# Optimization experiments

Hardware: AMD Instinct MI355X
Metric: run time of the kernel (lower is better)

## Reference

```python
import jax, jax.numpy as jnp
import numpy as np

N_BASIS = 5  # identity, transpose, diag-embed(diag), row-sum broadcast, total-sum broadcast


def eq2to2_ops(x):
    """x: [B, d, n, n] -> [B, 5, d, n, n] equivariant basis ops (sums normalized by n, n^2)."""
    n = x.shape[-1]
    eye = jnp.eye(n, dtype=x.dtype)
    xt = jnp.swapaxes(x, -1, -2)
    diag = jnp.diagonal(x, axis1=-2, axis2=-1)            # [B, d, n]
    diag_emb = diag[..., :, None] * eye                   # [B, d, n, n]
    row = jnp.broadcast_to(x.sum(-1, keepdims=True) / n, x.shape)
    tot = jnp.broadcast_to(x.sum((-2, -1), keepdims=True) / (n * n), x.shape)
    return jnp.stack([x, xt, diag_emb, row, tot], axis=1)


def eq_layer(x, W, b):
    """x: [B, d_in, n, n]; W: [d_in, d_out, 5]; b: [d_out] -> [B, d_out, n, n]."""
    ops = eq2to2_ops(x)                                   # [B, 5, d_in, n, n]
    return jnp.einsum('bqdij,dsq->bsij', ops, W) + b[None, :, None, None]


def setup_inputs() -> dict:
    key = jax.random.key(0)
    ks = jax.random.split(key, 8)
    B, n, nin, nhid, ndechid, nout = 8, 256, 16, 32, 128, 1
    s = lambda fan: 1.0 / np.sqrt(fan)
    return {
        'x': jax.random.normal(ks[0], (B, n, nin), jnp.float32),
        'W1': jax.random.normal(ks[1], (2 * nin, nhid, N_BASIS), jnp.float32) * s(2 * nin * N_BASIS),
        'b1': jnp.zeros((nhid,), jnp.float32),
        'W2': jax.random.normal(ks[2], (nhid, nhid, N_BASIS), jnp.float32) * s(nhid * N_BASIS),
        'b2': jnp.zeros((nhid,), jnp.float32),
        'D1': jax.random.normal(ks[3], (nhid, ndechid), jnp.float32) * s(nhid),
        'db1': jnp.zeros((ndechid,), jnp.float32),
        'D2': jax.random.normal(ks[4], (ndechid, ndechid), jnp.float32) * s(ndechid),
        'db2': jnp.zeros((ndechid,), jnp.float32),
        'D3': jax.random.normal(ks[5], (ndechid, nout), jnp.float32) * s(ndechid),
        'db3': jnp.zeros((nout,), jnp.float32),
    }


def reference(x, W1, b1, W2, b2, D1, db1, D2, db2, D3, db3):
    B, n, d = x.shape
    eye = jnp.eye(n, dtype=x.dtype)
    # diag_embed(x.permute(0,2,1)) -> [B, d, n, n]
    x1 = jnp.swapaxes(x, 1, 2)[..., :, None] * eye
    # outer-product pairwise interactions -> [B, d, n, n]
    x2 = jnp.einsum('bid,bjd->bdij', x, x)
    h = jnp.concatenate([x1, x2], axis=1)                 # [B, 2d, n, n]
    h = jax.nn.relu(eq_layer(h, W1, b1))
    h = jax.nn.relu(eq_layer(h, W2, b2))
    h = jax.nn.relu(h.sum((-2, -1)))                      # [B, nhid]
    h = jax.nn.relu(h @ D1 + db1)
    h = jax.nn.relu(h @ D2 + db2)
    return h @ D3 + db3
```

## Files before the change

kernel.cpp:

```cpp
#include <hip/hip_runtime.h>
#include <hip/hip_bf16.h>


#define NB 8
#define NN 256
#define ND 16
#define NC 32
#define W1S 160
#define W2S 160
#define XP 20

using bf16x8 = __attribute__((ext_vector_type(8))) __bf16;
using f32x4  = __attribute__((ext_vector_type(4))) float;

#define MFMA(a, b, c) __builtin_amdgcn_mfma_f32_16x16x32_bf16((a), (b), (c), 0, 0, 0)

#define WAVE_LDS_SYNC() do {                      \
    __builtin_amdgcn_wave_barrier();              \
    __builtin_amdgcn_s_waitcnt(0xc07f);  \
    __builtin_amdgcn_wave_barrier();              \
} while (0)

__device__ __forceinline__ bf16x8 make_av(const float* xi, const float* xj, int quad)
{
    bf16x8 av;
    if (quad < 2) {
        const float4* a = (const float4*)(xi + quad * 8);
        const float4* b = (const float4*)(xj + quad * 8);
        float4 a0 = a[0], a1 = a[1], b0 = b[0], b1 = b[1];
        av[0] = (__bf16)(a0.x * b0.x); av[1] = (__bf16)(a0.y * b0.y);
        av[2] = (__bf16)(a0.z * b0.z); av[3] = (__bf16)(a0.w * b0.w);
        av[4] = (__bf16)(a1.x * b1.x); av[5] = (__bf16)(a1.y * b1.y);
        av[6] = (__bf16)(a1.z * b1.z); av[7] = (__bf16)(a1.w * b1.w);
    } else {
        #pragma unroll
        for (int j = 0; j < 8; ++j) av[j] = (__bf16)0.f;
    }
    return av;
}

__device__ __forceinline__ unsigned pack2(float lo, float hi)
{
    union { __bf16 b[2]; unsigned u; } p;
    p.b[0] = (__bf16)lo; p.b[1] = (__bf16)hi;
    return p.u;
}

__global__ __launch_bounds__(256) void kC_rows(
    const float* __restrict__ x, const float* __restrict__ W1,
    const float* __restrict__ b1, const float* __restrict__ W2,
    float* __restrict__ T1g, float* __restrict__ R1, float* __restrict__ Dg1,
    float* __restrict__ TotP, float* __restrict__ CD2, float* __restrict__ CR2)
{
    const int TI = blockIdx.x, b = blockIdx.y, t = threadIdx.x;
    __shared__ __align__(16) float  sX[NN][XP];
    __shared__ __align__(16) __bf16 sBQ[NC][48];
    __shared__ float part[16][ND + 1];
    __shared__ float sS[ND];
    __shared__ float sRT[4][NC], sDgL[4][NC], sRow[4][NC], sDiag[4][NC];

    {
        const float4* xg4 = (const float4*)(x + b * NN * ND);
        #pragma unroll
        for (int kk = 0; kk < 4; ++kk) {
            int idx = t + kk * 256;
            int row = idx >> 2, c4 = idx & 3;
            *(float4*)&sX[row][c4 * 4] = xg4[idx];
        }
    }
    #pragma unroll
    for (int kk = 0; kk < 2; ++kk) {
        int idx = t + kk * 256; int c = idx >> 4, k = idx & 15;
        sBQ[c][k] = (__bf16)(W1[(ND + k) * W1S + c * 5 + 0]
                           + W1[(ND + k) * W1S + c * 5 + 1]);
    }
    #pragma unroll
    for (int kk = 0; kk < 4; ++kk) {
        int idx = t + kk * 256;
        sBQ[idx >> 5][16 + (idx & 31)] = (__bf16)0.f;
    }
    __syncthreads();

    {
        int rr = t >> 4, d = t & 15;
        float p = 0.f;
        #pragma unroll
        for (int k = 0; k < 16; ++k) p += sX[rr + (k << 4)][d];
        part[rr][d] = p;
    }
    __syncthreads();
    if (t < ND) {
        float s = 0.f;
        #pragma unroll
        for (int k = 0; k < 16; ++k) s += part[k][t];
        sS[t] = s;
    }
    __syncthreads();
    if (t < 128) {
        int i_l = t >> 5, c = t & 31;
        int gi = TI * 4 + i_l;
        float r = 0.f, dg = 0.f, tt = 0.f;
        #pragma unroll
        for (int d = 0; d < ND; ++d) {
            float xi = sX[gi][d], sd = sS[d];
            const float* wa = W1 + d * W1S + c * 5;
            const float* wb = W1 + (ND + d) * W1S + c * 5;
            r  += xi * wa[3] + xi * sd * wb[3];
            dg += xi * (wa[0] + wa[1] + wa[2]) + xi * xi * wb[2];
            tt += sd * wa[4] + sd * sd * wb[4];
        }
        r *= (1.f / 256.f);
        float t1 = tt * (1.f / 65536.f) + b1[c];
        R1[(b * NN + gi) * NC + c] = r;
        Dg1[(b * NN + gi) * NC + c] = dg;
        sRT[i_l][c] = t1 + r;
        sDgL[i_l][c] = dg;
        if (TI == 0 && i_l == 0) T1g[b * NC + c] = t1;
    }
    __syncthreads();

    const int ln = t & 63, wv = t >> 6;
    const int m = ln & 15, quad = ln >> 4;
    const int gi = TI * 4 + wv;
    bf16x8 bq0 = *(const bf16x8*)&sBQ[m][8 * quad];
    bf16x8 bq1 = *(const bf16x8*)&sBQ[m + 16][8 * quad];
    float rt0 = sRT[wv][m], rt1 = sRT[wv][m + 16];
    float dg0 = sDgL[wv][m], dg1 = sDgL[wv][m + 16];
    f32x4 zero = {0.f, 0.f, 0.f, 0.f};
    float rs0 = 0.f, rs1 = 0.f;

    for (int jg = 0; jg < 8; ++jg) {
        #pragma unroll
        for (int gg = 0; gg < 2; ++gg) {
            int jrow = jg * 32 + gg * 16 + m;
            bf16x8 av = make_av(&sX[gi][0], &sX[jrow][0], quad);
            f32x4 q0 = MFMA(av, bq0, zero);
            f32x4 q1 = MFMA(av, bq1, zero);
            int jb = jg * 32 + gg * 16 + quad * 4;
            #pragma unroll
            for (int r = 0; r < 4; ++r) {
                float v0 = q0[r] + rt0, v1 = q1[r] + rt1;
                bool dgf = (jb + r == gi);
                if (dgf) { v0 += dg0; v1 += dg1; }
                float h0 = fmaxf(v0, 0.f), h1 = fmaxf(v1, 0.f);
                if (dgf) { sDiag[wv][m] = h0; sDiag[wv][m + 16] = h1; }
                rs0 += h0; rs1 += h1;
            }
        }
    }
    rs0 += __shfl_down(rs0, 32, 64); rs0 += __shfl_down(rs0, 16, 64);
    rs1 += __shfl_down(rs1, 32, 64); rs1 += __shfl_down(rs1, 16, 64);
    if (ln < 16) { sRow[wv][ln] = rs0; sRow[wv][ln + 16] = rs1; }
    __syncthreads();
    if (t < NC)
        TotP[TI * (NB * NC) + b * NC + t]
            = sRow[0][t] + sRow[1][t] + sRow[2][t] + sRow[3][t];
    if (t < 128) {
        int i_l = t >> 5, s = t & 31;
        int gi2 = TI * 4 + i_l;
        float cd = 0.f, cr = 0.f;
        #pragma unroll
        for (int c = 0; c < NC; ++c) {
            cd += sDiag[i_l][c] * W2[c * W2S + s * 5 + 2];
            cr += sRow[i_l][c]  * W2[c * W2S + s * 5 + 3];
        }
        CD2[(b * NN + gi2) * NC + s] = cd;
        CR2[(b * NN + gi2) * NC + s] = cr * (1.f / 256.f);
    }
}

__global__ __launch_bounds__(256) void kD_main(
    const float* __restrict__ x, const float* __restrict__ W1,
    const float* __restrict__ W2, const float* __restrict__ b2,
    const float* __restrict__ T1g, const float* __restrict__ R1g,
    const float* __restrict__ Dg1g, const float* __restrict__ CD2g,
    const float* __restrict__ CR2g, const float* __restrict__ TotP,
    float* __restrict__ GP)
{
    const int b = blockIdx.y, t = threadIdx.x;
    int TI = 0, rem = blockIdx.x;
    while (rem >= 16 - TI) { rem -= 16 - TI; ++TI; }
    const int TJ = TI + rem;
    const bool diagblk = (TI == TJ), mirror = !diagblk;

    __shared__ __align__(16) __bf16 sUw[4][16][40];
    __shared__ __align__(16) __bf16 sVw[4][16][40];
    __shared__ __align__(16) __bf16 sBQ[NC][48];
    __shared__ __align__(16) __bf16 sWp[NC][40], sWm[NC][40];
    __shared__ __align__(16) float sXI[16][XP], sXJ[16][XP];
    __shared__ float sTot[NC], sCT2[NC];
    __shared__ float red[4][NC];

    if (t < 128) {
        const float4* xg4 = (const float4*)(x + b * NN * ND);
        int half = t >> 6, idx = t & 63;
        int row = idx >> 2, c4 = idx & 3;
        int base = (half ? TJ : TI) * 16;
        float4 v = xg4[(base + row) * 4 + c4];
        float* dst = half ? &sXJ[row][c4 * 4] : &sXI[row][c4 * 4];
        *(float4*)dst = v;
    }
    #pragma unroll
    for (int kk = 0; kk < 2; ++kk) {
        int idx = t + kk * 256; int c = idx >> 4, k = idx & 15;
        sBQ[c][k] = (__bf16)(W1[(ND + k) * W1S + c * 5 + 0]
                           + W1[(ND + k) * W1S + c * 5 + 1]);
    }
    #pragma unroll
    for (int kk = 0; kk < 4; ++kk) {
        int idx = t + kk * 256;
        sBQ[idx >> 5][16 + (idx & 31)] = (__bf16)0.f;
    }
    #pragma unroll
    for (int kk = 0; kk < 4; ++kk) {
        int idx = t + kk * 256; int s = idx >> 5, kp = idx & 31;
        int c = ((kp & 1) << 4) | (kp >> 1);
        float w0 = W2[c * W2S + s * 5 + 0], w1 = W2[c * W2S + s * 5 + 1];
        sWp[s][kp] = (__bf16)((w0 + w1) * 0.5f);
        sWm[s][kp] = (__bf16)((w0 - w1) * 0.5f);
    }
    if (t < NC) {
        float tot = 0.f;
        #pragma unroll
        for (int k = 0; k < 64; ++k) tot += TotP[k * (NB * NC) + b * NC + t];
        sTot[t] = tot;
    }
    if (t < 64) {
        WAVE_LDS_SYNC();
        if (t < NC) {
            float ct = 0.f;
            #pragma unroll
            for (int c = 0; c < NC; ++c) ct += sTot[c] * W2[c * W2S + t * 5 + 4];
            sCT2[t] = ct * (1.f / 65536.f) + b2[t];
        }
    }

    const int ln = t & 63, wv = t >> 6;
    const int m = ln & 15, quad = ln >> 4;

    const float* R1b = R1g + b * NN * NC;
    const float* Dgb = Dg1g + b * NN * NC;
    const float* CDb = CD2g + b * NN * NC;
    const float* CRb = CR2g + b * NN * NC;
    float t10 = T1g[b * NC + m], t11 = T1g[b * NC + m + 16];
    float rti[4][2], dgi[4][2], rtj[4][2];
    float cri[4][2], cdi[4][2], crj[4][2];
    #pragma unroll
    for (int gg = 0; gg < 4; ++gg) {
        int rowI = TI * 16 + wv * 4 + gg;
        rti[gg][0] = R1b[rowI * NC + m] + t10;
        rti[gg][1] = R1b[rowI * NC + m + 16] + t11;
        dgi[gg][0] = Dgb[rowI * NC + m];
        dgi[gg][1] = Dgb[rowI * NC + m + 16];
        cri[gg][0] = CRb[rowI * NC + m];
        cri[gg][1] = CRb[rowI * NC + m + 16];
        cdi[gg][0] = CDb[rowI * NC + m];
        cdi[gg][1] = CDb[rowI * NC + m + 16];
    }
    #pragma unroll
    for (int r = 0; r < 4; ++r) {
        int rowJ = TJ * 16 + quad * 4 + r;
        rtj[r][0] = R1b[rowJ * NC + m] + t10;
        rtj[r][1] = R1b[rowJ * NC + m + 16] + t11;
        crj[r][0] = CRb[rowJ * NC + m];
        crj[r][1] = CRb[rowJ * NC + m + 16];
    }
    __syncthreads();

    float ct0 = sCT2[m], ct1 = sCT2[m + 16];
    #pragma unroll
    for (int gg = 0; gg < 4; ++gg) { cri[gg][0] += ct0; cri[gg][1] += ct1; }
    #pragma unroll
    for (int r = 0; r < 4; ++r) { crj[r][0] += ct0; crj[r][1] += ct1; }

    bf16x8 bq0 = *(const bf16x8*)&sBQ[m][8 * quad];
    bf16x8 bq1 = *(const bf16x8*)&sBQ[m + 16][8 * quad];
    bf16x8 wp0 = *(const bf16x8*)&sWp[m][8 * quad];
    bf16x8 wp1 = *(const bf16x8*)&sWp[m + 16][8 * quad];
    bf16x8 wm0 = *(const bf16x8*)&sWm[m][8 * quad];
    bf16x8 wm1 = *(const bf16x8*)&sWm[m + 16][8 * quad];
    __bf16* Uw = &sUw[wv][0][0];
    __bf16* Vw = &sVw[wv][0][0];
    f32x4 zero = {0.f, 0.f, 0.f, 0.f};
    float acc0 = 0.f, acc1 = 0.f;

    #pragma unroll
    for (int gg = 0; gg < 4; ++gg) {
        int g = wv * 4 + gg;
        __builtin_amdgcn_wave_barrier();
        {
            bf16x8 av = make_av(&sXI[g][0], &sXJ[m][0], quad);
            f32x4 q0 = MFMA(av, bq0, zero);
            f32x4 q1 = MFMA(av, bq1, zero);
            #pragma unroll
            for (int r = 0; r < 4; ++r) {
                int tj = quad * 4 + r;
                float a0 = q0[r] + rti[gg][0], b0 = q0[r] + rtj[r][0];
                float a1 = q1[r] + rti[gg][1], b1 = q1[r] + rtj[r][1];
                if (diagblk && tj == g) {
                    a0 += dgi[gg][0]; b0 = a0;
                    a1 += dgi[gg][1]; b1 = a1;
                }
                float hA0 = fmaxf(a0, 0.f), hB0 = fmaxf(b0, 0.f);
                float hA1 = fmaxf(a1, 0.f), hB1 = fmaxf(b1, 0.f);
                *(unsigned*)&Uw[tj * 40 + 2 * m] = pack2(hA0 + hB0, hA1 + hB1);
                *(unsigned*)&Vw[tj * 40 + 2 * m] = pack2(hA0 - hB0, hA1 - hB1);
            }
        }
        WAVE_LDS_SYNC();
        {
            bf16x8 ua = *(const bf16x8*)&Uw[m * 40 + 8 * quad];
            bf16x8 va = *(const bf16x8*)&Vw[m * 40 + 8 * quad];
            f32x4 P0 = MFMA(ua, wp0, zero);
            f32x4 M0 = MFMA(va, wm0, zero);
            f32x4 P1 = MFMA(ua, wp1, zero);
            f32x4 M1 = MFMA(va, wm1, zero);
            #pragma unroll
            for (int r = 0; r < 4; ++r) {
                int tj = quad * 4 + r;
                float a1v = P0[r] + M0[r] + cri[gg][0];
                float a2v = P0[r] - M0[r] + crj[r][0];
                float e1 = P1[r] + M1[r] + cri[gg][1];
                float e2 = P1[r] - M1[r] + crj[r][1];
                if (diagblk && tj == g) { a1v += cdi[gg][0]; e1 += cdi[gg][1]; }
                acc0 += fmaxf(a1v, 0.f); acc1 += fmaxf(e1, 0.f);
                if (mirror) { acc0 += fmaxf(a2v, 0.f); acc1 += fmaxf(e2, 0.f); }
            }
        }
    }

    acc0 += __shfl_down(acc0, 32, 64); acc0 += __shfl_down(acc0, 16, 64);
    acc1 += __shfl_down(acc1, 32, 64); acc1 += __shfl_down(acc1, 16, 64);
    if (ln < 16) { red[wv][ln] = acc0; red[wv][ln + 16] = acc1; }
    __syncthreads();
    if (t < NC)
        GP[blockIdx.x * (NB * NC) + b * NC + t]
            = red[0][t] + red[1][t] + red[2][t] + red[3][t];
}

__global__ __launch_bounds__(256) void k5_mlp(
    const float* __restrict__ GP, const float* __restrict__ D1,
    const float* __restrict__ db1, const float* __restrict__ D2,
    const float* __restrict__ db2, const float* __restrict__ D3,
    const float* __restrict__ db3, float* __restrict__ out)
{
    int b = blockIdx.x, t = threadIdx.x;
    __shared__ float sGp[8][NC], a[NC], h2s[128], r2[2];
    {
        int q = t >> 5, s = t & 31;
        float p = 0.f;
        for (int k = q; k < 136; k += 8) p += GP[k * (NB * NC) + b * NC + s];
        sGp[q][s] = p;
    }
    __syncthreads();
    if (t < NC) {
        float s = 0.f;
        #pragma unroll
        for (int q = 0; q < 8; ++q) s += sGp[q][t];
        a[t] = fmaxf(s, 0.f);
    }
    __syncthreads();
    if (t < 128) {
        float acc = db1[t];
        #pragma unroll
        for (int s = 0; s < NC; ++s) acc += a[s] * D1[s * 128 + t];
        h2s[t] = fmaxf(acc, 0.f);
    }
    __syncthreads();
    if (t < 128) {
        float acc2 = db2[t];
        #pragma unroll 8
        for (int u = 0; u < 128; ++u) acc2 += h2s[u] * D2[u * 128 + t];
        float h3 = fmaxf(acc2, 0.f);
        float v = h3 * D3[t];
        #pragma unroll
        for (int off = 32; off > 0; off >>= 1) v += __shfl_down(v, off, 64);
        if ((t & 63) == 0) r2[t >> 6] = v;
    }
    __syncthreads();
    if (t == 0) out[b] = r2[0] + r2[1] + db3[0];
}

extern "C" void kernel_launch(void* const* d_in, const int* in_sizes, int n_in,
                              void* d_out, int out_size, void* d_ws, size_t ws_size,
                              hipStream_t stream)
{
    const float* x   = (const float*)d_in[0];
    const float* W1  = (const float*)d_in[1];
    const float* b1  = (const float*)d_in[2];
    const float* W2  = (const float*)d_in[3];
    const float* b2  = (const float*)d_in[4];
    const float* D1  = (const float*)d_in[5];
    const float* db1 = (const float*)d_in[6];
    const float* D2  = (const float*)d_in[7];
    const float* db2 = (const float*)d_in[8];
    const float* D3  = (const float*)d_in[9];
    const float* db3 = (const float*)d_in[10];
    float* out = (float*)d_out;

    float* w = (float*)d_ws;
    float* pT1   = w; w += NB * NC;
    float* pTotP = w; w += 64 * NB * NC;
    float* pGP   = w; w += 136 * NB * NC;
    float* pR1   = w; w += NB * NN * NC;
    float* pDg1  = w; w += NB * NN * NC;
    float* pCD2  = w; w += NB * NN * NC;
    float* pCR2  = w; w += NB * NN * NC;

    hipLaunchKernelGGL(kC_rows, dim3(64, NB), dim3(256), 0, stream,
                       x, W1, b1, W2, pT1, pR1, pDg1, pTotP, pCD2, pCR2);
    hipLaunchKernelGGL(kD_main, dim3(136, NB), dim3(256), 0, stream,
                       x, W1, W2, b2, pT1, pR1, pDg1, pCD2, pCR2, pTotP, pGP);
    hipLaunchKernelGGL(k5_mlp, dim3(NB), dim3(256), 0, stream,
                       pGP, D1, db1, D2, db2, D3, db3, out);
}
```

Before: 111.2 us.

## Fuse MLP tail into main kernel via last-block counter, precompute weight tiles

Removes the separate k5_mlp launch. The last block per batch to finish kD_main, detected with an atomic counter and release/acquire fences, now runs the MLP tail. The first kC_rows block precomputes the packed bf16 weight tiles (BQ, Wp/Wm, W2 slice 4) into workspace, so each kD_main block loads them with vector copies instead of rebuilding them from strided W2/W1 reads. kC_rows also stages W1 in shared memory for its per-row reductions. This adds atomics and a serialized tail in one block per batch, and extra shared memory in kC_rows.

```diff
diff --git a/kernel.cpp b/kernel.cpp
--- a/kernel.cpp
+++ b/kernel.cpp
@@ -9,6 +9,7 @@
 #define W1S 160
 #define W2S 160
 #define XP 20
+#define NBLK 136
 
 using bf16x8 = __attribute__((ext_vector_type(8))) __bf16;
 using f32x4  = __attribute__((ext_vector_type(4))) float;
@@ -50,10 +51,13 @@
     const float* __restrict__ x, const float* __restrict__ W1,
     const float* __restrict__ b1, const float* __restrict__ W2,
     float* __restrict__ T1g, float* __restrict__ R1, float* __restrict__ Dg1,
-    float* __restrict__ TotP, float* __restrict__ CD2, float* __restrict__ CR2)
+    float* __restrict__ TotP, float* __restrict__ CD2, float* __restrict__ CR2,
+    __bf16* __restrict__ BQt, __bf16* __restrict__ Wpm,
+    float* __restrict__ Wt4, int* __restrict__ Cnt)
 {
     const int TI = blockIdx.x, b = blockIdx.y, t = threadIdx.x;
     __shared__ __align__(16) float  sX[NN][XP];
+    __shared__ __align__(16) float  sW1[2 * ND][W1S];
     __shared__ __align__(16) __bf16 sBQ[NC][48];
     __shared__ float part[16][ND + 1];
     __shared__ float sS[ND];
@@ -68,6 +72,12 @@
             *(float4*)&sX[row][c4 * 4] = xg4[idx];
         }
     }
+    {
+        const float4* wg1 = (const float4*)W1;
+        float4* sw1 = (float4*)&sW1[0][0];
+        #pragma unroll
+        for (int kk = 0; kk < 5; ++kk) sw1[t + kk * 256] = wg1[t + kk * 256];
+    }
     #pragma unroll
     for (int kk = 0; kk < 2; ++kk) {
         int idx = t + kk * 256; int c = idx >> 4, k = idx & 15;
@@ -88,6 +98,19 @@
         for (int k = 0; k < 16; ++k) p += sX[rr + (k << 4)][d];
         part[rr][d] = p;
     }
+    if (TI == 0 && b == 0) {
+        if (t < 192) ((float4*)BQt)[t] = ((const float4*)&sBQ[0][0])[t];
+        for (int idx = t; idx < 1024; idx += 256) {
+            int s = idx >> 5, kp = idx & 31;
+            int c = ((kp & 1) << 4) | (kp >> 1);
+            float w0 = W2[c * W2S + s * 5 + 0], w1 = W2[c * W2S + s * 5 + 1];
+            Wpm[s * 40 + kp]        = (__bf16)((w0 + w1) * 0.5f);
+            Wpm[1280 + s * 40 + kp] = (__bf16)((w0 - w1) * 0.5f);
+        }
+        for (int idx = t; idx < 1024; idx += 256)
+            Wt4[(idx >> 5) * 32 + (idx & 31)] = W2[(idx >> 5) * W2S + (idx & 31) * 5 + 4];
+        if (t < NB) Cnt[t] = 0;
+    }
     __syncthreads();
     if (t < ND) {
         float s = 0.f;
@@ -103,8 +126,8 @@
         #pragma unroll
         for (int d = 0; d < ND; ++d) {
             float xi = sX[gi][d], sd = sS[d];
-            const float* wa = W1 + d * W1S + c * 5;
-            const float* wb = W1 + (ND + d) * W1S + c * 5;
+            const float* wa = &sW1[d][c * 5];
+            const float* wb = &sW1[ND + d][c * 5];
             r  += xi * wa[3] + xi * sd * wb[3];
             dg += xi * (wa[0] + wa[1] + wa[2]) + xi * xi * wb[2];
             tt += sd * wa[4] + sd * sd * wb[4];
@@ -170,12 +193,17 @@
 }
 
 __global__ __launch_bounds__(256) void kD_main(
-    const float* __restrict__ x, const float* __restrict__ W1,
-    const float* __restrict__ W2, const float* __restrict__ b2,
+    const float* __restrict__ x,
+    const __bf16* __restrict__ BQt, const __bf16* __restrict__ Wpm,
+    const float* __restrict__ Wt4, const float* __restrict__ b2,
     const float* __restrict__ T1g, const float* __restrict__ R1g,
     const float* __restrict__ Dg1g, const float* __restrict__ CD2g,
     const float* __restrict__ CR2g, const float* __restrict__ TotP,
-    float* __restrict__ GP)
+    float* __restrict__ GP, int* __restrict__ Cnt,
+    const float* __restrict__ D1, const float* __restrict__ db1,
+    const float* __restrict__ D2, const float* __restrict__ db2,
+    const float* __restrict__ D3, const float* __restrict__ db3,
+    float* __restrict__ out)
 {
     const int b = blockIdx.y, t = threadIdx.x;
     int TI = 0, rem = blockIdx.x;
@@ -190,6 +218,8 @@
     __shared__ __align__(16) float sXI[16][XP], sXJ[16][XP];
     __shared__ float sTot[NC], sCT2[NC];
     __shared__ float red[4][NC];
+    __shared__ int sLast;
+    __shared__ float sGp[8][NC], sA[NC], h2s[128], r2[2];
 
     if (t < 128) {
         const float4* xg4 = (const float4*)(x + b * NN * ND);
@@ -200,24 +230,15 @@
         float* dst = half ? &sXJ[row][c4 * 4] : &sXI[row][c4 * 4];
         *(float4*)dst = v;
     }
-    #pragma unroll
-    for (int kk = 0; kk < 2; ++kk) {
-        int idx = t + kk * 256; int c = idx >> 4, k = idx & 15;
-        sBQ[c][k] = (__bf16)(W1[(ND + k) * W1S + c * 5 + 0]
-                           + W1[(ND + k) * W1S + c * 5 + 1]);
-    }
-    #pragma unroll
-    for (int kk = 0; kk < 4; ++kk) {
-        int idx = t + kk * 256;
-        sBQ[idx >> 5][16 + (idx & 31)] = (__bf16)0.f;
-    }
-    #pragma unroll
-    for (int kk = 0; kk < 4; ++kk) {
-        int idx = t + kk * 256; int s = idx >> 5, kp = idx & 31;
-        int c = ((kp & 1) << 4) | (kp >> 1);
-        float w0 = W2[c * W2S + s * 5 + 0], w1 = W2[c * W2S + s * 5 + 1];
-        sWp[s][kp] = (__bf16)((w0 + w1) * 0.5f);
-        sWm[s][kp] = (__bf16)((w0 - w1) * 0.5f);
+    if (t < 192) ((float4*)&sBQ[0][0])[t] = ((const float4*)BQt)[t];
+    {
+        const float4* wsrc = (const float4*)Wpm;
+        #pragma unroll
+        for (int i = t; i < 320; i += 256) {
+            float4 v = wsrc[i];
+            if (i < 160) ((float4*)&sWp[0][0])[i] = v;
+            else         ((float4*)&sWm[0][0])[i - 160] = v;
+        }
     }
     if (t < NC) {
         float tot = 0.f;
@@ -230,7 +251,7 @@
         if (t < NC) {
             float ct = 0.f;
             #pragma unroll
-            for (int c = 0; c < NC; ++c) ct += sTot[c] * W2[c * W2S + t * 5 + 4];
+            for (int c = 0; c < NC; ++c) ct += sTot[c] * Wt4[c * 32 + t];
             sCT2[t] = ct * (1.f / 65536.f) + b2[t];
         }
     }
@@ -336,20 +357,24 @@
     if (t < NC)
         GP[blockIdx.x * (NB * NC) + b * NC + t]
             = red[0][t] + red[1][t] + red[2][t] + red[3][t];
-}
-
-__global__ __launch_bounds__(256) void k5_mlp(
-    const float* __restrict__ GP, const float* __restrict__ D1,
-    const float* __restrict__ db1, const float* __restrict__ D2,
-    const float* __restrict__ db2, const float* __restrict__ D3,
-    const float* __restrict__ db3, float* __restrict__ out)
-{
-    int b = blockIdx.x, t = threadIdx.x;
-    __shared__ float sGp[8][NC], a[NC], h2s[128], r2[2];
+
+    __builtin_amdgcn_fence(__ATOMIC_RELEASE, "agent");
+    if (t == 0) {
+        int old = __hip_atomic_fetch_add(Cnt + b, 1, __ATOMIC_RELAXED,
+                                         __HIP_MEMORY_SCOPE_AGENT);
+        sLast = (old == NBLK - 1) ? 1 : 0;
+    }
+    __syncthreads();
+    if (!sLast) return;
+    __builtin_amdgcn_fence(__ATOMIC_ACQUIRE, "agent");
+
     {
         int q = t >> 5, s = t & 31;
         float p = 0.f;
-        for (int k = q; k < 136; k += 8) p += GP[k * (NB * NC) + b * NC + s];
+        #pragma unroll
+        for (int k = q; k < NBLK; k += 8)
+            p += __hip_atomic_load(&GP[k * (NB * NC) + b * NC + s],
+                                   __ATOMIC_RELAXED, __HIP_MEMORY_SCOPE_AGENT);
         sGp[q][s] = p;
     }
     __syncthreads();
@@ -357,13 +382,13 @@
         float s = 0.f;
         #pragma unroll
         for (int q = 0; q < 8; ++q) s += sGp[q][t];
-        a[t] = fmaxf(s, 0.f);
+        sA[t] = fmaxf(s, 0.f);
     }
     __syncthreads();
     if (t < 128) {
         float acc = db1[t];
         #pragma unroll
-        for (int s = 0; s < NC; ++s) acc += a[s] * D1[s * 128 + t];
+        for (int s = 0; s < NC; ++s) acc += sA[s] * D1[s * 128 + t];
         h2s[t] = fmaxf(acc, 0.f);
     }
     __syncthreads();
@@ -401,16 +426,20 @@
     float* w = (float*)d_ws;
     float* pT1   = w; w += NB * NC;
     float* pTotP = w; w += 64 * NB * NC;
-    float* pGP   = w; w += 136 * NB * NC;
+    float* pGP   = w; w += NBLK * NB * NC;
     float* pR1   = w; w += NB * NN * NC;
     float* pDg1  = w; w += NB * NN * NC;
     float* pCD2  = w; w += NB * NN * NC;
     float* pCR2  = w; w += NB * NN * NC;
+    __bf16* pBQt = (__bf16*)w; w += 768;
+    __bf16* pWpm = (__bf16*)w; w += 1280;
+    float* pWt4  = w; w += 1024;
+    int*   pCnt  = (int*)w; w += 8;
 
     hipLaunchKernelGGL(kC_rows, dim3(64, NB), dim3(256), 0, stream,
-                       x, W1, b1, W2, pT1, pR1, pDg1, pTotP, pCD2, pCR2);
-    hipLaunchKernelGGL(kD_main, dim3(136, NB), dim3(256), 0, stream,
-                       x, W1, W2, b2, pT1, pR1, pDg1, pCD2, pCR2, pTotP, pGP);
-    hipLaunchKernelGGL(k5_mlp, dim3(NB), dim3(256), 0, stream,
-                       pGP, D1, db1, D2, db2, D3, db3, out);
+                       x, W1, b1, W2, pT1, pR1, pDg1, pTotP, pCD2, pCR2,
+                       pBQt, pWpm, pWt4, pCnt);
+    hipLaunchKernelGGL(kD_main, dim3(NBLK, NB), dim3(256), 0, stream,
+                       x, pBQt, pWpm, pWt4, b2, pT1, pR1, pDg1, pCD2, pCR2,
+                       pTotP, pGP, pCnt, D1, db1, D2, db2, D3, db3, out);
 }
```

Measured after the change: 145.4 us. 30.8% more time.
